# Optimization experiments

Measured on AMD Instinct MI355X. Metric: run time of the kernel, lower is better.

Reference implementation:

```python
import jax, jax.numpy as jnp
import numpy as np

B, C, H, W = 8, 16, 256, 256
HID = 32

def setup_inputs() -> dict:
    key = jax.random.key(0)
    ks = jax.random.split(key, 6)
    swin_logits = jax.random.normal(ks[0], (B, C, H, W), dtype=jnp.float32)
    gru_logits = jax.random.normal(ks[1], (B, C, H, W), dtype=jnp.float32)
    # per-class gate params (stacked across classes); torch Linear default-ish scale
    W1 = jax.random.normal(ks[2], (C, HID, 2), dtype=jnp.float32) * (1.0 / np.sqrt(2.0))
    b1 = jax.random.normal(ks[3], (C, HID), dtype=jnp.float32) * 0.1
    W2 = jax.random.normal(ks[4], (C, 2, HID), dtype=jnp.float32) * (1.0 / np.sqrt(HID))
    b2 = jax.random.normal(ks[5], (C, 2), dtype=jnp.float32) * 0.1
    # expert_preferences initialized exactly as in the torch module
    pref = np.zeros((C, 2), dtype=np.float32)
    for i in range(C):
        w_hls = 0.3 + 0.4 * (i / max(1, C - 1))
        pref[i] = [w_hls, 1.0 - w_hls]
    expert_preferences = jnp.asarray(pref)
    return {"swin_logits": swin_logits, "gru_logits": gru_logits,
            "W1": W1, "b1": b1, "W2": W2, "b2": b2,
            "expert_preferences": expert_preferences}

def reference(swin_logits, gru_logits, W1, b1, W2, b2, expert_preferences):
    b, c, h, w = swin_logits.shape
    # class-dim softmax over logits
    swin_probs = jax.nn.softmax(swin_logits, axis=1)
    gru_probs = jax.nn.softmax(gru_logits, axis=1)
    # (B,C,H,W) -> (N,C), N = B*H*W
    sp = swin_probs.transpose(0, 2, 3, 1).reshape(-1, c)
    gp = gru_probs.transpose(0, 2, 3, 1).reshape(-1, c)
    gate_in = jnp.stack([sp, gp], axis=-1)  # (N, C, 2)
    # batched per-class gate MLP (Dropout is identity in eval mode)
    hid = jax.nn.relu(jnp.einsum('nci,chi->nch', gate_in, W1) + b1)  # (N,C,HID)
    dynamic_weights = jax.nn.softmax(jnp.einsum('nch,coh->nco', hid, W2) + b2, axis=-1)  # (N,C,2)
    # weighted fusion of expert logits
    sl = swin_logits.transpose(0, 2, 3, 1).reshape(-1, c)
    gl = gru_logits.transpose(0, 2, 3, 1).reshape(-1, c)
    expert_logits = jnp.stack([sl, gl], axis=-1)  # (N,C,2)
    fused_flat = jnp.sum(dynamic_weights * expert_logits, axis=-1)  # (N,C)
    fused_logits = fused_flat.reshape(b, h, w, c).transpose(0, 3, 1, 2)
    return fused_logits, expert_preferences, dynamic_weights
```

## Files before the change

kernel.cpp:

```cpp
#include <hip/hip_runtime.h>

typedef float v2f __attribute__((ext_vector_type(2)));

#define Bc   8
#define Cc   16
#define HWc  65536
#define HIDc 32
#define Npix (Bc * HWc)
#define FUSED_ELEMS (Bc * Cc * HWc)
#define PREF_ELEMS  (Cc * 2)
#define TPB  256
#define WSTRIDE 81
#define PACKED_BYTES (Cc * WSTRIDE * 8)

__global__ void gate_prep(const float* __restrict__ W1, const float* __restrict__ b1,
                          const float* __restrict__ W2, const float* __restrict__ b2,
                          v2f* __restrict__ ws)
{
    const int c = blockIdx.x;
    const int j = threadIdx.x;
    v2f* wp = ws + c * WSTRIDE;
    if (j < 16) {
        wp[j]      = (v2f){W1[c*64 + 4*j + 0], W1[c*64 + 4*j + 2]};
        wp[16 + j] = (v2f){W1[c*64 + 4*j + 1], W1[c*64 + 4*j + 3]};
        wp[32 + j] = (v2f){b1[c*32 + 2*j],     b1[c*32 + 2*j + 1]};
        wp[48 + j] = (v2f){W2[c*64 + 2*j],     W2[c*64 + 2*j + 1]};
        wp[64 + j] = (v2f){W2[c*64 + 32 + 2*j],W2[c*64 + 32 + 2*j + 1]};
    } else if (j == 16) {
        wp[80] = (v2f){b2[2*c], b2[2*c + 1]};
    }
}

__global__ __launch_bounds__(TPB)
__attribute__((amdgpu_waves_per_eu(4, 4)))
void gate_main_packed(
    const float* __restrict__ swin, const float* __restrict__ gru,
    const v2f* __restrict__ wsw, const float* __restrict__ pref,
    float* __restrict__ out)
{
    __shared__ float2 dwbuf2[TPB * Cc];

    const int tid  = threadIdx.x;
    const int n    = blockIdx.x * TPB + tid;
    const int bidx = n >> 16;
    const int hw   = n & (HWc - 1);

    const float* sptr = swin + (size_t)bidx * (Cc * HWc) + hw;
    const float* gptr = gru  + (size_t)bidx * (Cc * HWc) + hw;

    float sl[Cc], gl[Cc];
#pragma unroll
    for (int c = 0; c < Cc; ++c) {
        sl[c] = sptr[c * HWc];
        gl[c] = gptr[c * HWc];
    }

    float ms = sl[0], mg = gl[0];
#pragma unroll
    for (int c = 1; c < Cc; ++c) {
        ms = fmaxf(ms, sl[c]);
        mg = fmaxf(mg, gl[c]);
    }
    float es[Cc], eg[Cc];
    float ss = 0.f, sg = 0.f;
#pragma unroll
    for (int c = 0; c < Cc; ++c) {
        es[c] = __expf(sl[c] - ms);  ss += es[c];
        eg[c] = __expf(gl[c] - mg);  sg += eg[c];
    }
    const float invs = __builtin_amdgcn_rcpf(ss);
    const float invg = __builtin_amdgcn_rcpf(sg);

    float* fop = out + (size_t)bidx * (Cc * HWc) + hw;

#pragma unroll
    for (int c = 0; c < Cc; ++c) {
        const float sp = es[c] * invs;
        const float gp = eg[c] * invg;
        const v2f spv = {sp, sp};
        const v2f gpv = {gp, gp};

        const v2f* wp = wsw + c * WSTRIDE;

        v2f acc0 = {0.f, 0.f};
        v2f acc1 = {0.f, 0.f};
#pragma unroll
        for (int j = 0; j < HIDc / 2; ++j) {
            v2f h = wp[j] * spv + (wp[16 + j] * gpv + wp[32 + j]);
            h = __builtin_elementwise_max(h, (v2f){0.f, 0.f});
            acc0 = h * wp[48 + j] + acc0;
            acc1 = h * wp[64 + j] + acc1;
        }
        const v2f b2v = wp[80];
        const float a0 = acc0.x + acc0.y + b2v.x;
        const float a1 = acc1.x + acc1.y + b2v.y;

        const float d = a0 - a1;
        const float t = __expf(-fabsf(d));
        const float r = __builtin_amdgcn_rcpf(1.f + t);
        const float w0 = (d >= 0.f) ? r : 1.f - r;
        const float w1 = 1.f - w0;

        fop[c * HWc] = fmaf(w0, sl[c], w1 * gl[c]);

        dwbuf2[tid * Cc + ((c + tid) & (Cc - 1))] = make_float2(w0, w1);
    }

    __syncthreads();

    float2* outv2 = reinterpret_cast<float2*>(
        out + (size_t)FUSED_ELEMS + PREF_ELEMS + (size_t)blockIdx.x * (TPB * Cc * 2));
#pragma unroll
    for (int j = 0; j < Cc; ++j) {
        const int pi = j * TPB + tid;
        const int p  = pi >> 4;
        const int pr = pi & (Cc - 1);
        outv2[pi] = dwbuf2[p * Cc + ((pr + p) & (Cc - 1))];
    }

    if (blockIdx.x == 0 && tid < PREF_ELEMS) {
        out[(size_t)FUSED_ELEMS + tid] = pref[tid];
    }
}

__global__ __launch_bounds__(TPB, 4) void gate_main_scalar(
    const float* __restrict__ swin, const float* __restrict__ gru,
    const float* __restrict__ W1, const float* __restrict__ b1,
    const float* __restrict__ W2, const float* __restrict__ b2,
    const float* __restrict__ pref, float* __restrict__ out)
{
    __shared__ float2 dwbuf2[TPB * Cc];

    const int tid  = threadIdx.x;
    const int n    = blockIdx.x * TPB + tid;
    const int bidx = n >> 16;
    const int hw   = n & (HWc - 1);

    const float* sptr = swin + (size_t)bidx * (Cc * HWc) + hw;
    const float* gptr = gru  + (size_t)bidx * (Cc * HWc) + hw;

    float sl[Cc], gl[Cc];
#pragma unroll
    for (int c = 0; c < Cc; ++c) { sl[c] = sptr[c * HWc]; gl[c] = gptr[c * HWc]; }

    float ms = sl[0], mg = gl[0];
#pragma unroll
    for (int c = 1; c < Cc; ++c) { ms = fmaxf(ms, sl[c]); mg = fmaxf(mg, gl[c]); }
    float es[Cc], eg[Cc];
    float ss = 0.f, sg = 0.f;
#pragma unroll
    for (int c = 0; c < Cc; ++c) {
        es[c] = __expf(sl[c] - ms);  ss += es[c];
        eg[c] = __expf(gl[c] - mg);  sg += eg[c];
    }
    const float invs = __builtin_amdgcn_rcpf(ss);
    const float invg = __builtin_amdgcn_rcpf(sg);

    float* fop = out + (size_t)bidx * (Cc * HWc) + hw;

#pragma unroll
    for (int c = 0; c < Cc; ++c) {
        const float sp = es[c] * invs;
        const float gp = eg[c] * invg;
        const float* w1c = W1 + c * (HIDc * 2);
        const float* b1c = b1 + c * HIDc;
        const float* w2c = W2 + c * (2 * HIDc);

        float a0 = b2[c * 2 + 0];
        float a1 = b2[c * 2 + 1];
#pragma unroll
        for (int k = 0; k < HIDc; ++k) {
            float h = fmaf(w1c[k * 2 + 0], sp, fmaf(w1c[k * 2 + 1], gp, b1c[k]));
            h = fmaxf(h, 0.f);
            a0 = fmaf(w2c[k], h, a0);
            a1 = fmaf(w2c[HIDc + k], h, a1);
        }
        const float d = a0 - a1;
        const float t = __expf(-fabsf(d));
        const float r = __builtin_amdgcn_rcpf(1.f + t);
        const float w0 = (d >= 0.f) ? r : 1.f - r;
        const float w1 = 1.f - w0;

        fop[c * HWc] = fmaf(w0, sl[c], w1 * gl[c]);
        dwbuf2[tid * Cc + ((c + tid) & (Cc - 1))] = make_float2(w0, w1);
    }

    __syncthreads();

    float2* outv2 = reinterpret_cast<float2*>(
        out + (size_t)FUSED_ELEMS + PREF_ELEMS + (size_t)blockIdx.x * (TPB * Cc * 2));
#pragma unroll
    for (int j = 0; j < Cc; ++j) {
        const int pi = j * TPB + tid;
        const int p  = pi >> 4;
        const int pr = pi & (Cc - 1);
        outv2[pi] = dwbuf2[p * Cc + ((pr + p) & (Cc - 1))];
    }

    if (blockIdx.x == 0 && tid < PREF_ELEMS) {
        out[(size_t)FUSED_ELEMS + tid] = pref[tid];
    }
}

extern "C" void kernel_launch(void* const* d_in, const int* in_sizes, int n_in,
                              void* d_out, int out_size, void* d_ws, size_t ws_size,
                              hipStream_t stream) {
    const float* swin = (const float*)d_in[0];
    const float* gru  = (const float*)d_in[1];
    const float* W1   = (const float*)d_in[2];
    const float* b1   = (const float*)d_in[3];
    const float* W2   = (const float*)d_in[4];
    const float* b2   = (const float*)d_in[5];
    const float* pref = (const float*)d_in[6];
    float* out = (float*)d_out;

    dim3 grid(Npix / TPB);
    dim3 block(TPB);

    if (ws_size >= (size_t)PACKED_BYTES) {
        v2f* ws = (v2f*)d_ws;
        hipLaunchKernelGGL(gate_prep, dim3(Cc), dim3(64), 0, stream, W1, b1, W2, b2, ws);
        hipLaunchKernelGGL(gate_main_packed, grid, block, 0, stream,
                           swin, gru, ws, pref, out);
    } else {
        hipLaunchKernelGGL(gate_main_scalar, grid, block, 0, stream,
                           swin, gru, W1, b1, W2, b2, pref, out);
    }
}
```

Measured before the change: 198.7 us.

## Drop LDS transpose of gate weights, store directly, raise occupancy target

Removes the shared-memory staging buffer and barrier used to coalesce the dynamic-weight output. Each thread now writes its own 128 contiguous bytes as float4 pairs. The softmax drops max subtraction and recomputes exp per class instead of keeping the es/eg arrays, which frees registers so the waves-per-EU target can rise from 4 to 6-8. The cost is less coalesced stores, extra exp instructions, and a risk of overflow for large logits because the max shift is gone.

```diff
diff --git a/kernel.cpp b/kernel.cpp
--- a/kernel.cpp
+++ b/kernel.cpp
@@ -32,14 +32,12 @@
 }
 
 __global__ __launch_bounds__(TPB)
-__attribute__((amdgpu_waves_per_eu(4, 4)))
+__attribute__((amdgpu_waves_per_eu(6, 8)))
 void gate_main_packed(
     const float* __restrict__ swin, const float* __restrict__ gru,
     const v2f* __restrict__ wsw, const float* __restrict__ pref,
     float* __restrict__ out)
 {
-    __shared__ float2 dwbuf2[TPB * Cc];
-
     const int tid  = threadIdx.x;
     const int n    = blockIdx.x * TPB + tid;
     const int bidx = n >> 16;
@@ -55,28 +53,24 @@
         gl[c] = gptr[c * HWc];
     }
 
-    float ms = sl[0], mg = gl[0];
-#pragma unroll
-    for (int c = 1; c < Cc; ++c) {
-        ms = fmaxf(ms, sl[c]);
-        mg = fmaxf(mg, gl[c]);
-    }
-    float es[Cc], eg[Cc];
-    float ss = 0.f, sg = 0.f;
-#pragma unroll
-    for (int c = 0; c < Cc; ++c) {
-        es[c] = __expf(sl[c] - ms);  ss += es[c];
-        eg[c] = __expf(gl[c] - mg);  sg += eg[c];
-    }
-    const float invs = __builtin_amdgcn_rcpf(ss);
-    const float invg = __builtin_amdgcn_rcpf(sg);
+    float ss0 = 0.f, ss1 = 0.f, sg0 = 0.f, sg1 = 0.f;
+#pragma unroll
+    for (int c = 0; c < Cc; c += 2) {
+        ss0 += __expf(sl[c]);     sg0 += __expf(gl[c]);
+        ss1 += __expf(sl[c + 1]); sg1 += __expf(gl[c + 1]);
+    }
+    const float invs = __builtin_amdgcn_rcpf(ss0 + ss1);
+    const float invg = __builtin_amdgcn_rcpf(sg0 + sg1);
 
     float* fop = out + (size_t)bidx * (Cc * HWc) + hw;
-
-#pragma unroll
-    for (int c = 0; c < Cc; ++c) {
-        const float sp = es[c] * invs;
-        const float gp = eg[c] * invg;
+    float4* dwp = reinterpret_cast<float4*>(
+        out + (size_t)FUSED_ELEMS + PREF_ELEMS + (size_t)n * (Cc * 2));
+
+    float w0e = 0.f, w1e = 0.f;
+#pragma unroll
+    for (int c = 0; c < Cc; ++c) {
+        const float sp = __expf(sl[c]) * invs;
+        const float gp = __expf(gl[c]) * invg;
         const v2f spv = {sp, sp};
         const v2f gpv = {gp, gp};
 
@@ -103,19 +97,12 @@
 
         fop[c * HWc] = fmaf(w0, sl[c], w1 * gl[c]);
 
-        dwbuf2[tid * Cc + ((c + tid) & (Cc - 1))] = make_float2(w0, w1);
-    }
-
-    __syncthreads();
-
-    float2* outv2 = reinterpret_cast<float2*>(
-        out + (size_t)FUSED_ELEMS + PREF_ELEMS + (size_t)blockIdx.x * (TPB * Cc * 2));
-#pragma unroll
-    for (int j = 0; j < Cc; ++j) {
-        const int pi = j * TPB + tid;
-        const int p  = pi >> 4;
-        const int pr = pi & (Cc - 1);
-        outv2[pi] = dwbuf2[p * Cc + ((pr + p) & (Cc - 1))];
+        if (c & 1) {
+            dwp[c >> 1] = make_float4(w0e, w1e, w0, w1);
+        } else {
+            w0e = w0;
+            w1e = w1;
+        }
     }
 
     if (blockIdx.x == 0 && tid < PREF_ELEMS) {
```

New measurement: 233.6 us. +17.6%, slower.
